# Optimization experiments

Hardware: AMD Instinct MI355X
Metric: run time of the kernel (lower is better)

## Reference

```python
import jax, jax.numpy as jnp
import numpy as np

N_NODES = 50000
N_EDGES = 800000
C_IN = 128
HEADS = 4
C_HEAD = 32  # c_out // heads = 128 // 4
NEG_SLOPE = 0.2


def setup_inputs() -> dict:
    key = jax.random.key(0)
    k_x, k_e, k_w, k_as, k_ad, k_b = jax.random.split(key, 6)
    x = jax.random.normal(k_x, (N_NODES, C_IN), dtype=jnp.float32)
    edge_index = jax.random.randint(k_e, (2, N_EDGES), 0, N_NODES, dtype=jnp.int64)
    # xavier_uniform_ with gain=1.414 on lin.weight [H*C, C_IN] -> same bound for W [C_IN, H*C]
    bound = 1.414 * np.sqrt(6.0 / (C_IN + HEADS * C_HEAD))
    W = jax.random.uniform(k_w, (C_IN, HEADS * C_HEAD), minval=-bound, maxval=bound, dtype=jnp.float32)
    # glorot init for attention vectors (PyG default)
    ab = np.sqrt(6.0 / (1 + HEADS * C_HEAD))
    att_src = jax.random.uniform(k_as, (HEADS, C_HEAD), minval=-ab, maxval=ab, dtype=jnp.float32)
    att_dst = jax.random.uniform(k_ad, (HEADS, C_HEAD), minval=-ab, maxval=ab, dtype=jnp.float32)
    bias = jnp.zeros((HEADS * C_HEAD,), dtype=jnp.float32)
    return {"x": x, "edge_index": edge_index, "W": W,
            "att_src": att_src, "att_dst": att_dst, "bias": bias}


def reference(x, edge_index, W, att_src, att_dst, bias):
    N = x.shape[0]
    H, C = att_src.shape
    # Linear projection, per-head split: [N, H, C]
    xl = (x @ W).reshape(N, H, C)
    a_src = jnp.einsum('nhc,hc->nh', xl, att_src)  # [N, H]
    a_dst = jnp.einsum('nhc,hc->nh', xl, att_dst)  # [N, H]

    src, dst = edge_index[0], edge_index[1]
    loop = jnp.arange(N, dtype=edge_index.dtype)
    # GATConv(add_self_loops=True): remove existing self loops, then add one per node.
    src_f = jnp.concatenate([src, loop])  # [E+N]
    dst_f = jnp.concatenate([dst, loop])
    drop = jnp.concatenate([src == dst, jnp.zeros((N,), dtype=bool)])

    e = jax.nn.leaky_relu(a_src[src_f] + a_dst[dst_f], NEG_SLOPE)  # [E+N, H]
    e = jnp.where(drop[:, None], -jnp.inf, e)

    # segment softmax over edges sharing a destination (every node has a self loop -> max is finite)
    m = jax.ops.segment_max(e, dst_f, num_segments=N)          # [N, H]
    ex = jnp.exp(e - m[dst_f])                                  # [E+N, H]
    denom = jax.ops.segment_sum(ex, dst_f, num_segments=N)     # [N, H]
    alpha = ex / denom[dst_f]                                   # [E+N, H]

    msg = xl[src_f] * alpha[:, :, None]                         # [E+N, H, C]
    out = jax.ops.segment_sum(msg, dst_f, num_segments=N)      # [N, H, C]
    out = out.reshape(N, H * C) + bias
    return out / jnp.sqrt(jnp.asarray(H, dtype=out.dtype))
```

## Files before the change

kernel.cpp:

```cpp
#include <hip/hip_runtime.h>
#include <math.h>

#define CDIM 128
#define HEADS 4
#define NEG 0.2f
#define BSTRIDE 64

typedef __attribute__((ext_vector_type(8))) short bf16x8;
typedef __attribute__((ext_vector_type(8))) unsigned short u16x8;
typedef __attribute__((ext_vector_type(4))) float f32x4;

static __device__ __forceinline__ unsigned short f2bf(float f) {
    unsigned u = __float_as_uint(f);
    u += 0x7FFFu + ((u >> 16) & 1u);
    return (unsigned short)(u >> 16);
}
static __device__ __forceinline__ float bf2f(unsigned short s) {
    return __uint_as_float((unsigned)s << 16);
}

static __device__ __forceinline__ void accum8(float* acc, float w, u16x8 u) {
    const unsigned* pw = (const unsigned*)&u;
#pragma unroll
    for (int i = 0; i < 4; ++i) {
        unsigned wd = pw[i];
        acc[2 * i]     = fmaf(w, __uint_as_float(wd << 16), acc[2 * i]);
        acc[2 * i + 1] = fmaf(w, __uint_as_float(wd & 0xFFFF0000u), acc[2 * i + 1]);
    }
}

#define LDS_STRIDE 136

__global__ __launch_bounds__(256) void wt_kernel(const float* __restrict__ W,
                                                 unsigned short* __restrict__ WT,
                                                 int* __restrict__ counts, int nClr) {
    int f = blockIdx.x * 256 + threadIdx.x;
    for (int i = f; i < nClr; i += 4096) counts[i] = 0;
    int k = f >> 5, c4 = (f & 31) * 4;
    float4 v = *(const float4*)(W + (size_t)k * CDIM + c4);
    WT[(size_t)(c4 + 0) * CDIM + k] = f2bf(v.x);
    WT[(size_t)(c4 + 1) * CDIM + k] = f2bf(v.y);
    WT[(size_t)(c4 + 2) * CDIM + k] = f2bf(v.z);
    WT[(size_t)(c4 + 3) * CDIM + k] = f2bf(v.w);
}

__global__ __launch_bounds__(256) void gemm_hist_kernel(const float* __restrict__ x,
                                                        const unsigned short* __restrict__ WT,
                                                        const float* __restrict__ att_src,
                                                        const float* __restrict__ att_dst,
                                                        unsigned short* __restrict__ xlh,
                                                        float* __restrict__ a_src,
                                                        float* __restrict__ a_dst, int N,
                                                        const int* __restrict__ esrc,
                                                        const int* __restrict__ edst,
                                                        int* __restrict__ counts,
                                                        unsigned* __restrict__ packed, int E,
                                                        int gemmBlocks) {
    __shared__ unsigned short As[64 * LDS_STRIDE];

    if ((int)blockIdx.x >= gemmBlocks) {
        int e = (blockIdx.x - gemmBlocks) * 256 + threadIdx.x;
        if (e < E) {
            int s = esrc[e], d = edst[e];
            unsigned pk = ~0u;
            if (s != d) {
                int r = atomicAdd(&counts[d], 1);
                pk = (unsigned)d | ((unsigned)r << 16);
            }
            packed[e] = pk;
        }
        return;
    }

    const int tid = threadIdx.x;
    const int row0 = blockIdx.x * 64;

#pragma unroll
    for (int i = 0; i < 8; ++i) {
        int f = tid + i * 256;
        int r = f >> 5, k4 = f & 31;
        float4 v = make_float4(0.f, 0.f, 0.f, 0.f);
        int gr = row0 + r;
        if (gr < N) v = *(const float4*)(x + (size_t)gr * CDIM + k4 * 4);
        ushort4 h;
        h.x = f2bf(v.x); h.y = f2bf(v.y); h.z = f2bf(v.z); h.w = f2bf(v.w);
        *(ushort4*)(&As[r * LDS_STRIDE + k4 * 4]) = h;
    }
    __syncthreads();

    const int wave = tid >> 6;
    const int lane = tid & 63;
    const int m    = lane & 15;
    const int quad = lane >> 4;
    const int wrow = wave * 16;

    bf16x8 a[4];
#pragma unroll
    for (int ks = 0; ks < 4; ++ks)
        a[ks] = *(const bf16x8*)(&As[(wrow + m) * LDS_STRIDE + ks * 32 + quad * 8]);

    f32x4 acc[8];
#pragma unroll
    for (int t = 0; t < 8; ++t) {
        f32x4 c = {0.f, 0.f, 0.f, 0.f};
#pragma unroll
        for (int ks = 0; ks < 4; ++ks) {
            bf16x8 b = *(const bf16x8*)(WT + (size_t)(t * 16 + m) * CDIM + ks * 32 + quad * 8);
            c = __builtin_amdgcn_mfma_f32_16x16x32_bf16(a[ks], b, c, 0, 0, 0);
        }
        acc[t] = c;
    }

#pragma unroll
    for (int t = 0; t < 8; ++t) {
#pragma unroll
        for (int reg = 0; reg < 4; ++reg) {
            int row = row0 + wrow + quad * 4 + reg;
            if (row < N) xlh[(size_t)row * CDIM + t * 16 + m] = f2bf(acc[t][reg]);
        }
    }

    float ps[4][4], pd[4][4];
#pragma unroll
    for (int h = 0; h < 4; ++h)
#pragma unroll
        for (int reg = 0; reg < 4; ++reg) { ps[h][reg] = 0.f; pd[h][reg] = 0.f; }
#pragma unroll
    for (int t = 0; t < 8; ++t) {
        int h = t >> 1;
        float vs = att_src[t * 16 + m];
        float vd = att_dst[t * 16 + m];
#pragma unroll
        for (int reg = 0; reg < 4; ++reg) {
            ps[h][reg] += acc[t][reg] * vs;
            pd[h][reg] += acc[t][reg] * vd;
        }
    }
#pragma unroll
    for (int off = 8; off > 0; off >>= 1) {
#pragma unroll
        for (int h = 0; h < 4; ++h)
#pragma unroll
            for (int reg = 0; reg < 4; ++reg) {
                ps[h][reg] += __shfl_down(ps[h][reg], off, 16);
                pd[h][reg] += __shfl_down(pd[h][reg], off, 16);
            }
    }
    if (m == 0) {
#pragma unroll
        for (int reg = 0; reg < 4; ++reg) {
            int row = row0 + wrow + quad * 4 + reg;
            if (row < N) {
#pragma unroll
                for (int h = 0; h < 4; ++h) {
                    a_src[row * 4 + h] = ps[h][reg];
                    a_dst[row * 4 + h] = pd[h][reg];
                }
            }
        }
    }
}

__global__ __launch_bounds__(256) void scatter_kernel(const int* __restrict__ src,
                                                      const unsigned* __restrict__ packed,
                                                      int* __restrict__ bucket, int E) {
    int base = (blockIdx.x * 256 + threadIdx.x) * 4;
    if (base + 4 <= E) {
        int4 s4 = *(const int4*)(src + base);
        uint4 p4 = *(const uint4*)(packed + base);
        int ss[4] = {s4.x, s4.y, s4.z, s4.w};
        unsigned pp[4] = {p4.x, p4.y, p4.z, p4.w};
#pragma unroll
        for (int q = 0; q < 4; ++q) {
            unsigned r = pp[q] >> 16;
            if (pp[q] != ~0u && r < BSTRIDE)
                bucket[(pp[q] & 0xFFFFu) * BSTRIDE + r] = ss[q];
        }
    } else {
        for (int e = base; e < E; ++e) {
            unsigned pk = packed[e];
            unsigned r = pk >> 16;
            if (pk != ~0u && r < BSTRIDE) bucket[(pk & 0xFFFFu) * BSTRIDE + r] = src[e];
        }
    }
}

__global__ __launch_bounds__(256) void gather_kernel(const int* __restrict__ counts,
                                                     const int* __restrict__ bucket,
                                                     const unsigned short* __restrict__ xlh,
                                                     const float* __restrict__ a_src,
                                                     const float* __restrict__ a_dst,
                                                     const float* __restrict__ bias,
                                                     float* __restrict__ out, int N) {
    const int node = blockIdx.x * 4 + (threadIdx.x >> 6);
    const int lane = threadIdx.x & 63;
    const int g = lane >> 4;
    const int lane16 = lane & 15;
    if (node >= N) return;
    const int c8 = lane16 * 8;
    const int h = lane16 >> 2;

    const float ad = a_dst[node * 4 + h];
    const int beg = node * BSTRIDE;
    int cnt = counts[node];
    if (cnt > BSTRIDE) cnt = BSTRIDE;

    float acc[8];
#pragma unroll
    for (int i = 0; i < 8; ++i) acc[i] = 0.f;
    float den = 0.f;

    int j = g;
    for (; j + 12 < cnt; j += 16) {
        int s[4];
#pragma unroll
        for (int q = 0; q < 4; ++q) s[q] = bucket[beg + j + 4 * q];
        float e[4];
#pragma unroll
        for (int q = 0; q < 4; ++q) e[q] = a_src[s[q] * 4 + h] + ad;
        u16x8 u[4];
#pragma unroll
        for (int q = 0; q < 4; ++q) u[q] = *(const u16x8*)(xlh + (size_t)s[q] * CDIM + c8);
        float w[4];
#pragma unroll
        for (int q = 0; q < 4; ++q) {
            float eq = e[q] > 0.f ? e[q] : NEG * e[q];
            w[q] = __expf(eq);
        }
#pragma unroll
        for (int q = 0; q < 4; ++q) {
            accum8(acc, w[q], u[q]);
            den += w[q];
        }
    }
    for (; j < cnt; j += 4) {
        int s = bucket[beg + j];
        float e = a_src[s * 4 + h] + ad;
        u16x8 u = *(const u16x8*)(xlh + (size_t)s * CDIM + c8);
        e = e > 0.f ? e : NEG * e;
        float w = __expf(e);
        accum8(acc, w, u);
        den += w;
    }
    if (g == 0) {
        float es = a_src[node * 4 + h] + ad;
        es = es > 0.f ? es : NEG * es;
        float ws = __expf(es);
        u16x8 u = *(const u16x8*)(xlh + (size_t)node * CDIM + c8);
        accum8(acc, ws, u);
        den += ws;
    }
#pragma unroll
    for (int i = 0; i < 8; ++i) {
        acc[i] += __shfl_xor(acc[i], 16);
        acc[i] += __shfl_xor(acc[i], 32);
    }
    den += __shfl_xor(den, 16);
    den += __shfl_xor(den, 32);

    if (g == 0) {
        float inv = 1.0f / den;
        float4 b0 = *(const float4*)(bias + c8);
        float4 b1 = *(const float4*)(bias + c8 + 4);
        float4 o0, o1;
        o0.x = (acc[0] * inv + b0.x) * 0.5f;
        o0.y = (acc[1] * inv + b0.y) * 0.5f;
        o0.z = (acc[2] * inv + b0.z) * 0.5f;
        o0.w = (acc[3] * inv + b0.w) * 0.5f;
        o1.x = (acc[4] * inv + b1.x) * 0.5f;
        o1.y = (acc[5] * inv + b1.y) * 0.5f;
        o1.z = (acc[6] * inv + b1.z) * 0.5f;
        o1.w = (acc[7] * inv + b1.w) * 0.5f;
        *(float4*)(out + (size_t)node * CDIM + c8) = o0;
        *(float4*)(out + (size_t)node * CDIM + c8 + 4) = o1;
    }
}

extern "C" void kernel_launch(void* const* d_in, const int* in_sizes, int n_in,
                              void* d_out, int out_size, void* d_ws, size_t ws_size,
                              hipStream_t stream) {
    const float* x       = (const float*)d_in[0];
    const int*   ei      = (const int*)d_in[1];
    const float* W       = (const float*)d_in[2];
    const float* att_src = (const float*)d_in[3];
    const float* att_dst = (const float*)d_in[4];
    const float* bias    = (const float*)d_in[5];
    float* out = (float*)d_out;

    const int N = in_sizes[0] / CDIM;
    const int E = in_sizes[1] / 2;

    char* wsb = (char*)d_ws;
    unsigned short* xlh = (unsigned short*)wsb;         wsb += (size_t)N * CDIM * sizeof(unsigned short);
    unsigned short* WT  = (unsigned short*)wsb;         wsb += (size_t)CDIM * CDIM * sizeof(unsigned short);
    float* a_src = (float*)wsb;                         wsb += (size_t)N * HEADS * sizeof(float);
    float* a_dst = (float*)wsb;                         wsb += (size_t)N * HEADS * sizeof(float);
    int* counts  = (int*)wsb;                           wsb += (size_t)N * sizeof(int);
    unsigned* packed = (unsigned*)wsb;                  wsb += (size_t)E * sizeof(unsigned);
    int* bucket  = (int*)wsb;                           wsb += (size_t)N * BSTRIDE * sizeof(int);

    wt_kernel<<<16, 256, 0, stream>>>(W, WT, counts, N);
    const int gemmBlocks = (N + 63) / 64;
    const int histBlocks = (E + 255) / 256;
    gemm_hist_kernel<<<gemmBlocks + histBlocks, 256, 0, stream>>>(
        x, WT, att_src, att_dst, xlh, a_src, a_dst, N, ei, ei + E, counts, packed, E, gemmBlocks);
    scatter_kernel<<<((E + 3) / 4 + 255) / 256, 256, 0, stream>>>(ei, packed, bucket, E);
    gather_kernel<<<(N + 3) / 4, 256, 0, stream>>>(counts, bucket, xlh, a_src, a_dst, bias, out, N);
}
```

Baseline: 169.8 us.

## Fuse all stages into one persistent cooperative kernel with grid syncs

Replaces the four separate launches (weight transpose, GEMM plus histogram, scatter, gather) with one persistent cooperative kernel. Grid-wide syncs separate the phases, and grid-stride loops cover the work. In the GEMM/histogram phase a fixed 40% of blocks run GEMM tiles while the rest do edge counting. The aim is to remove launch gaps and inter-kernel drain. The cost is grid-sync overhead, occupancy limited to resident blocks, and a static split that may leave work unbalanced.

```diff
diff --git a/kernel.cpp b/kernel.cpp
--- a/kernel.cpp
+++ b/kernel.cpp
@@ -1,5 +1,8 @@
 #include <hip/hip_runtime.h>
+#include <hip/hip_cooperative_groups.h>
 #include <math.h>
+
+namespace cg = cooperative_groups;
 
 #define CDIM 128
 #define HEADS 4
@@ -31,36 +34,132 @@
 
 #define LDS_STRIDE 136
 
-__global__ __launch_bounds__(256) void wt_kernel(const float* __restrict__ W,
-                                                 unsigned short* __restrict__ WT,
-                                                 int* __restrict__ counts, int nClr) {
-    int f = blockIdx.x * 256 + threadIdx.x;
-    for (int i = f; i < nClr; i += 4096) counts[i] = 0;
-    int k = f >> 5, c4 = (f & 31) * 4;
-    float4 v = *(const float4*)(W + (size_t)k * CDIM + c4);
-    WT[(size_t)(c4 + 0) * CDIM + k] = f2bf(v.x);
-    WT[(size_t)(c4 + 1) * CDIM + k] = f2bf(v.y);
-    WT[(size_t)(c4 + 2) * CDIM + k] = f2bf(v.z);
-    WT[(size_t)(c4 + 3) * CDIM + k] = f2bf(v.w);
-}
-
-__global__ __launch_bounds__(256) void gemm_hist_kernel(const float* __restrict__ x,
-                                                        const unsigned short* __restrict__ WT,
-                                                        const float* __restrict__ att_src,
-                                                        const float* __restrict__ att_dst,
-                                                        unsigned short* __restrict__ xlh,
-                                                        float* __restrict__ a_src,
-                                                        float* __restrict__ a_dst, int N,
-                                                        const int* __restrict__ esrc,
-                                                        const int* __restrict__ edst,
-                                                        int* __restrict__ counts,
-                                                        unsigned* __restrict__ packed, int E,
-                                                        int gemmBlocks) {
+__global__ __launch_bounds__(256) void mega_kernel(
+    const float* __restrict__ x, const float* __restrict__ W,
+    unsigned short* __restrict__ WT,
+    const float* __restrict__ att_src, const float* __restrict__ att_dst,
+    const float* __restrict__ bias,
+    unsigned short* __restrict__ xlh, float* __restrict__ a_src, float* __restrict__ a_dst,
+    int* __restrict__ counts, unsigned* __restrict__ packed,
+    int* __restrict__ bucket, float* __restrict__ out,
+    const int* __restrict__ esrc, const int* __restrict__ edst,
+    int N, int E, int gemmBlocks)
+{
     __shared__ unsigned short As[64 * LDS_STRIDE];
-
-    if ((int)blockIdx.x >= gemmBlocks) {
-        int e = (blockIdx.x - gemmBlocks) * 256 + threadIdx.x;
-        if (e < E) {
+    cg::grid_group grid = cg::this_grid();
+    const int b   = blockIdx.x;
+    const int tid = threadIdx.x;
+    const int gsz = gridDim.x;
+
+    {
+        int f = b * 256 + tid;
+        for (int i = f; i < N; i += gsz * 256) counts[i] = 0;
+        if (f < 4096) {
+            int k = f >> 5, c4 = (f & 31) * 4;
+            float4 v = *(const float4*)(W + (size_t)k * CDIM + c4);
+            WT[(size_t)(c4 + 0) * CDIM + k] = f2bf(v.x);
+            WT[(size_t)(c4 + 1) * CDIM + k] = f2bf(v.y);
+            WT[(size_t)(c4 + 2) * CDIM + k] = f2bf(v.z);
+            WT[(size_t)(c4 + 3) * CDIM + k] = f2bf(v.w);
+        }
+    }
+    grid.sync();
+
+    int gs25 = (gsz * 2) / 5;
+    int gemmSplit = gemmBlocks < gs25 ? gemmBlocks : gs25;
+    if (b < gemmSplit) {
+        for (int tile = b; tile < gemmBlocks; tile += gemmSplit) {
+            const int row0 = tile * 64;
+
+#pragma unroll
+            for (int i = 0; i < 8; ++i) {
+                int f = tid + i * 256;
+                int r = f >> 5, k4 = f & 31;
+                float4 v = make_float4(0.f, 0.f, 0.f, 0.f);
+                int gr = row0 + r;
+                if (gr < N) v = *(const float4*)(x + (size_t)gr * CDIM + k4 * 4);
+                ushort4 h;
+                h.x = f2bf(v.x); h.y = f2bf(v.y); h.z = f2bf(v.z); h.w = f2bf(v.w);
+                *(ushort4*)(&As[r * LDS_STRIDE + k4 * 4]) = h;
+            }
+            __syncthreads();
+
+            const int wave = tid >> 6;
+            const int lane = tid & 63;
+            const int m    = lane & 15;
+            const int quad = lane >> 4;
+            const int wrow = wave * 16;
+
+            bf16x8 a[4];
+#pragma unroll
+            for (int ks = 0; ks < 4; ++ks)
+                a[ks] = *(const bf16x8*)(&As[(wrow + m) * LDS_STRIDE + ks * 32 + quad * 8]);
+
+            f32x4 acc[8];
+#pragma unroll
+            for (int t = 0; t < 8; ++t) {
+                f32x4 c = {0.f, 0.f, 0.f, 0.f};
+#pragma unroll
+                for (int ks = 0; ks < 4; ++ks) {
+                    bf16x8 bb = *(const bf16x8*)(WT + (size_t)(t * 16 + m) * CDIM + ks * 32 + quad * 8);
+                    c = __builtin_amdgcn_mfma_f32_16x16x32_bf16(a[ks], bb, c, 0, 0, 0);
+                }
+                acc[t] = c;
+            }
+
+#pragma unroll
+            for (int t = 0; t < 8; ++t) {
+#pragma unroll
+                for (int reg = 0; reg < 4; ++reg) {
+                    int row = row0 + wrow + quad * 4 + reg;
+                    if (row < N) xlh[(size_t)row * CDIM + t * 16 + m] = f2bf(acc[t][reg]);
+                }
+            }
+
+            float ps[4][4], pd[4][4];
+#pragma unroll
+            for (int h = 0; h < 4; ++h)
+#pragma unroll
+                for (int reg = 0; reg < 4; ++reg) { ps[h][reg] = 0.f; pd[h][reg] = 0.f; }
+#pragma unroll
+            for (int t = 0; t < 8; ++t) {
+                int h = t >> 1;
+                float vs = att_src[t * 16 + m];
+                float vd = att_dst[t * 16 + m];
+#pragma unroll
+                for (int reg = 0; reg < 4; ++reg) {
+                    ps[h][reg] += acc[t][reg] * vs;
+                    pd[h][reg] += acc[t][reg] * vd;
+                }
+            }
+#pragma unroll
+            for (int off = 8; off > 0; off >>= 1) {
+#pragma unroll
+                for (int h = 0; h < 4; ++h)
+#pragma unroll
+                    for (int reg = 0; reg < 4; ++reg) {
+                        ps[h][reg] += __shfl_down(ps[h][reg], off, 16);
+                        pd[h][reg] += __shfl_down(pd[h][reg], off, 16);
+                    }
+            }
+            if (m == 0) {
+#pragma unroll
+                for (int reg = 0; reg < 4; ++reg) {
+                    int row = row0 + wrow + quad * 4 + reg;
+                    if (row < N) {
+#pragma unroll
+                        for (int h = 0; h < 4; ++h) {
+                            a_src[row * 4 + h] = ps[h][reg];
+                            a_dst[row * 4 + h] = pd[h][reg];
+                        }
+                    }
+                }
+            }
+            __syncthreads();
+        }
+    } else {
+        int stride = (gsz - gemmSplit) * 256;
+        for (int e = (b - gemmSplit) * 256 + tid; e < E; e += stride) {
             int s = esrc[e], d = edst[e];
             unsigned pk = ~0u;
             if (s != d) {
@@ -69,210 +168,121 @@
             }
             packed[e] = pk;
         }
-        return;
-    }
-
-    const int tid = threadIdx.x;
-    const int row0 = blockIdx.x * 64;
-
-#pragma unroll
-    for (int i = 0; i < 8; ++i) {
-        int f = tid + i * 256;
-        int r = f >> 5, k4 = f & 31;
-        float4 v = make_float4(0.f, 0.f, 0.f, 0.f);
-        int gr = row0 + r;
-        if (gr < N) v = *(const float4*)(x + (size_t)gr * CDIM + k4 * 4);
-        ushort4 h;
-        h.x = f2bf(v.x); h.y = f2bf(v.y); h.z = f2bf(v.z); h.w = f2bf(v.w);
-        *(ushort4*)(&As[r * LDS_STRIDE + k4 * 4]) = h;
-    }
-    __syncthreads();
-
-    const int wave = tid >> 6;
-    const int lane = tid & 63;
-    const int m    = lane & 15;
-    const int quad = lane >> 4;
-    const int wrow = wave * 16;
-
-    bf16x8 a[4];
-#pragma unroll
-    for (int ks = 0; ks < 4; ++ks)
-        a[ks] = *(const bf16x8*)(&As[(wrow + m) * LDS_STRIDE + ks * 32 + quad * 8]);
-
-    f32x4 acc[8];
-#pragma unroll
-    for (int t = 0; t < 8; ++t) {
-        f32x4 c = {0.f, 0.f, 0.f, 0.f};
-#pragma unroll
-        for (int ks = 0; ks < 4; ++ks) {
-            bf16x8 b = *(const bf16x8*)(WT + (size_t)(t * 16 + m) * CDIM + ks * 32 + quad * 8);
-            c = __builtin_amdgcn_mfma_f32_16x16x32_bf16(a[ks], b, c, 0, 0, 0);
-        }
-        acc[t] = c;
-    }
-
-#pragma unroll
-    for (int t = 0; t < 8; ++t) {
-#pragma unroll
-        for (int reg = 0; reg < 4; ++reg) {
-            int row = row0 + wrow + quad * 4 + reg;
-            if (row < N) xlh[(size_t)row * CDIM + t * 16 + m] = f2bf(acc[t][reg]);
-        }
-    }
-
-    float ps[4][4], pd[4][4];
-#pragma unroll
-    for (int h = 0; h < 4; ++h)
-#pragma unroll
-        for (int reg = 0; reg < 4; ++reg) { ps[h][reg] = 0.f; pd[h][reg] = 0.f; }
-#pragma unroll
-    for (int t = 0; t < 8; ++t) {
-        int h = t >> 1;
-        float vs = att_src[t * 16 + m];
-        float vd = att_dst[t * 16 + m];
-#pragma unroll
-        for (int reg = 0; reg < 4; ++reg) {
-            ps[h][reg] += acc[t][reg] * vs;
-            pd[h][reg] += acc[t][reg] * vd;
-        }
-    }
-#pragma unroll
-    for (int off = 8; off > 0; off >>= 1) {
-#pragma unroll
-        for (int h = 0; h < 4; ++h)
-#pragma unroll
-            for (int reg = 0; reg < 4; ++reg) {
-                ps[h][reg] += __shfl_down(ps[h][reg], off, 16);
-                pd[h][reg] += __shfl_down(pd[h][reg], off, 16);
-            }
-    }
-    if (m == 0) {
-#pragma unroll
-        for (int reg = 0; reg < 4; ++reg) {
-            int row = row0 + wrow + quad * 4 + reg;
-            if (row < N) {
-#pragma unroll
-                for (int h = 0; h < 4; ++h) {
-                    a_src[row * 4 + h] = ps[h][reg];
-                    a_dst[row * 4 + h] = pd[h][reg];
-                }
-            }
-        }
-    }
-}
-
-__global__ __launch_bounds__(256) void scatter_kernel(const int* __restrict__ src,
-                                                      const unsigned* __restrict__ packed,
-                                                      int* __restrict__ bucket, int E) {
-    int base = (blockIdx.x * 256 + threadIdx.x) * 4;
-    if (base + 4 <= E) {
-        int4 s4 = *(const int4*)(src + base);
-        uint4 p4 = *(const uint4*)(packed + base);
-        int ss[4] = {s4.x, s4.y, s4.z, s4.w};
-        unsigned pp[4] = {p4.x, p4.y, p4.z, p4.w};
-#pragma unroll
-        for (int q = 0; q < 4; ++q) {
-            unsigned r = pp[q] >> 16;
-            if (pp[q] != ~0u && r < BSTRIDE)
-                bucket[(pp[q] & 0xFFFFu) * BSTRIDE + r] = ss[q];
-        }
-    } else {
-        for (int e = base; e < E; ++e) {
-            unsigned pk = packed[e];
-            unsigned r = pk >> 16;
-            if (pk != ~0u && r < BSTRIDE) bucket[(pk & 0xFFFFu) * BSTRIDE + r] = src[e];
-        }
-    }
-}
-
-__global__ __launch_bounds__(256) void gather_kernel(const int* __restrict__ counts,
-                                                     const int* __restrict__ bucket,
-                                                     const unsigned short* __restrict__ xlh,
-                                                     const float* __restrict__ a_src,
-                                                     const float* __restrict__ a_dst,
-                                                     const float* __restrict__ bias,
-                                                     float* __restrict__ out, int N) {
-    const int node = blockIdx.x * 4 + (threadIdx.x >> 6);
-    const int lane = threadIdx.x & 63;
-    const int g = lane >> 4;
-    const int lane16 = lane & 15;
-    if (node >= N) return;
-    const int c8 = lane16 * 8;
-    const int h = lane16 >> 2;
-
-    const float ad = a_dst[node * 4 + h];
-    const int beg = node * BSTRIDE;
-    int cnt = counts[node];
-    if (cnt > BSTRIDE) cnt = BSTRIDE;
-
-    float acc[8];
-#pragma unroll
-    for (int i = 0; i < 8; ++i) acc[i] = 0.f;
-    float den = 0.f;
-
-    int j = g;
-    for (; j + 12 < cnt; j += 16) {
-        int s[4];
-#pragma unroll
-        for (int q = 0; q < 4; ++q) s[q] = bucket[beg + j + 4 * q];
-        float e[4];
-#pragma unroll
-        for (int q = 0; q < 4; ++q) e[q] = a_src[s[q] * 4 + h] + ad;
-        u16x8 u[4];
-#pragma unroll
-        for (int q = 0; q < 4; ++q) u[q] = *(const u16x8*)(xlh + (size_t)s[q] * CDIM + c8);
-        float w[4];
-#pragma unroll
-        for (int q = 0; q < 4; ++q) {
-            float eq = e[q] > 0.f ? e[q] : NEG * e[q];
-            w[q] = __expf(eq);
-        }
-#pragma unroll
-        for (int q = 0; q < 4; ++q) {
-            accum8(acc, w[q], u[q]);
-            den += w[q];
-        }
-    }
-    for (; j < cnt; j += 4) {
-        int s = bucket[beg + j];
-        float e = a_src[s * 4 + h] + ad;
-        u16x8 u = *(const u16x8*)(xlh + (size_t)s * CDIM + c8);
-        e = e > 0.f ? e : NEG * e;
-        float w = __expf(e);
-        accum8(acc, w, u);
-        den += w;
-    }
-    if (g == 0) {
-        float es = a_src[node * 4 + h] + ad;
-        es = es > 0.f ? es : NEG * es;
-        float ws = __expf(es);
-        u16x8 u = *(const u16x8*)(xlh + (size_t)node * CDIM + c8);
-        accum8(acc, ws, u);
-        den += ws;
-    }
-#pragma unroll
-    for (int i = 0; i < 8; ++i) {
-        acc[i] += __shfl_xor(acc[i], 16);
-        acc[i] += __shfl_xor(acc[i], 32);
-    }
-    den += __shfl_xor(den, 16);
-    den += __shfl_xor(den, 32);
-
-    if (g == 0) {
-        float inv = 1.0f / den;
-        float4 b0 = *(const float4*)(bias + c8);
-        float4 b1 = *(const float4*)(bias + c8 + 4);
-        float4 o0, o1;
-        o0.x = (acc[0] * inv + b0.x) * 0.5f;
-        o0.y = (acc[1] * inv + b0.y) * 0.5f;
-        o0.z = (acc[2] * inv + b0.z) * 0.5f;
-        o0.w = (acc[3] * inv + b0.w) * 0.5f;
-        o1.x = (acc[4] * inv + b1.x) * 0.5f;
-        o1.y = (acc[5] * inv + b1.y) * 0.5f;
-        o1.z = (acc[6] * inv + b1.z) * 0.5f;
-        o1.w = (acc[7] * inv + b1.w) * 0.5f;
-        *(float4*)(out + (size_t)node * CDIM + c8) = o0;
-        *(float4*)(out + (size_t)node * CDIM + c8 + 4) = o1;
+    }
+    grid.sync();
+
+    {
+        int nchunk = (E + 3) / 4;
+        for (int c = b * 256 + tid; c < nchunk; c += gsz * 256) {
+            int base = c * 4;
+            if (base + 4 <= E) {
+                int4 s4 = *(const int4*)(esrc + base);
+                uint4 p4 = *(const uint4*)(packed + base);
+                int ss[4] = {s4.x, s4.y, s4.z, s4.w};
+                unsigned pp[4] = {p4.x, p4.y, p4.z, p4.w};
+#pragma unroll
+                for (int q = 0; q < 4; ++q) {
+                    unsigned r = pp[q] >> 16;
+                    if (pp[q] != ~0u && r < BSTRIDE)
+                        bucket[(pp[q] & 0xFFFFu) * BSTRIDE + r] = ss[q];
+                }
+            } else {
+                for (int e = base; e < E; ++e) {
+                    unsigned pk = packed[e];
+                    unsigned r = pk >> 16;
+                    if (pk != ~0u && r < BSTRIDE) bucket[(pk & 0xFFFFu) * BSTRIDE + r] = esrc[e];
+                }
+            }
+        }
+    }
+    grid.sync();
+
+    {
+        int nquad = (N + 3) / 4;
+        for (int qd = b; qd < nquad; qd += gsz) {
+            const int node = qd * 4 + (tid >> 6);
+            if (node >= N) continue;
+            const int lane = tid & 63;
+            const int g = lane >> 4;
+            const int lane16 = lane & 15;
+            const int c8 = lane16 * 8;
+            const int h = lane16 >> 2;
+
+            const float ad = a_dst[node * 4 + h];
+            const int beg = node * BSTRIDE;
+            int cnt = counts[node];
+            if (cnt > BSTRIDE) cnt = BSTRIDE;
+
+            float acc[8];
+#pragma unroll
+            for (int i = 0; i < 8; ++i) acc[i] = 0.f;
+            float den = 0.f;
+
+            int j = g;
+            for (; j + 12 < cnt; j += 16) {
+                int s[4];
+#pragma unroll
+                for (int q = 0; q < 4; ++q) s[q] = bucket[beg + j + 4 * q];
+                float e[4];
+#pragma unroll
+                for (int q = 0; q < 4; ++q) e[q] = a_src[s[q] * 4 + h] + ad;
+                u16x8 u[4];
+#pragma unroll
+                for (int q = 0; q < 4; ++q) u[q] = *(const u16x8*)(xlh + (size_t)s[q] * CDIM + c8);
+                float w[4];
+#pragma unroll
+                for (int q = 0; q < 4; ++q) {
+                    float eq = e[q] > 0.f ? e[q] : NEG * e[q];
+                    w[q] = __expf(eq);
+                }
+#pragma unroll
+                for (int q = 0; q < 4; ++q) {
+                    accum8(acc, w[q], u[q]);
+                    den += w[q];
+                }
+            }
+            for (; j < cnt; j += 4) {
+                int s = bucket[beg + j];
+                float e = a_src[s * 4 + h] + ad;
+                u16x8 u = *(const u16x8*)(xlh + (size_t)s * CDIM + c8);
+                e = e > 0.f ? e : NEG * e;
+                float w = __expf(e);
+                accum8(acc, w, u);
+                den += w;
+            }
+            if (g == 0) {
+                float es = a_src[node * 4 + h] + ad;
+                es = es > 0.f ? es : NEG * es;
+                float ws = __expf(es);
+                u16x8 u = *(const u16x8*)(xlh + (size_t)node * CDIM + c8);
+                accum8(acc, ws, u);
+                den += ws;
+            }
+#pragma unroll
+            for (int i = 0; i < 8; ++i) {
+                acc[i] += __shfl_xor(acc[i], 16);
+                acc[i] += __shfl_xor(acc[i], 32);
+            }
+            den += __shfl_xor(den, 16);
+            den += __shfl_xor(den, 32);
+
+            if (g == 0) {
+                float inv = 1.0f / den;
+                float4 b0 = *(const float4*)(bias + c8);
+                float4 b1 = *(const float4*)(bias + c8 + 4);
+                float4 o0, o1;
+                o0.x = (acc[0] * inv + b0.x) * 0.5f;
+                o0.y = (acc[1] * inv + b0.y) * 0.5f;
+                o0.z = (acc[2] * inv + b0.z) * 0.5f;
+                o0.w = (acc[3] * inv + b0.w) * 0.5f;
+                o1.x = (acc[4] * inv + b1.x) * 0.5f;
+                o1.y = (acc[5] * inv + b1.y) * 0.5f;
+                o1.z = (acc[6] * inv + b1.z) * 0.5f;
+                o1.w = (acc[7] * inv + b1.w) * 0.5f;
+                *(float4*)(out + (size_t)node * CDIM + c8) = o0;
+                *(float4*)(out + (size_t)node * CDIM + c8 + 4) = o1;
+            }
+        }
     }
 }
 
@@ -287,8 +297,8 @@
     const float* bias    = (const float*)d_in[5];
     float* out = (float*)d_out;
 
-    const int N = in_sizes[0] / CDIM;
-    const int E = in_sizes[1] / 2;
+    int N = in_sizes[0] / CDIM;
+    int E = in_sizes[1] / 2;
 
     char* wsb = (char*)d_ws;
     unsigned short* xlh = (unsigned short*)wsb;         wsb += (size_t)N * CDIM * sizeof(unsigned short);
@@ -299,11 +309,27 @@
     unsigned* packed = (unsigned*)wsb;                  wsb += (size_t)E * sizeof(unsigned);
     int* bucket  = (int*)wsb;                           wsb += (size_t)N * BSTRIDE * sizeof(int);
 
-    wt_kernel<<<16, 256, 0, stream>>>(W, WT, counts, N);
-    const int gemmBlocks = (N + 63) / 64;
-    const int histBlocks = (E + 255) / 256;
-    gemm_hist_kernel<<<gemmBlocks + histBlocks, 256, 0, stream>>>(
-        x, WT, att_src, att_dst, xlh, a_src, a_dst, N, ei, ei + E, counts, packed, E, gemmBlocks);
-    scatter_kernel<<<((E + 3) / 4 + 255) / 256, 256, 0, stream>>>(ei, packed, bucket, E);
-    gather_kernel<<<(N + 3) / 4, 256, 0, stream>>>(counts, bucket, xlh, a_src, a_dst, bias, out, N);
-}
+    static int gridBlocks = 0;
+    if (gridBlocks == 0) {
+        int nbPerCU = 0;
+        if (hipOccupancyMaxActiveBlocksPerMultiprocessor(&nbPerCU, mega_kernel, 256, 0) != hipSuccess
+            || nbPerCU <= 0)
+            nbPerCU = 4;
+        int cus = 256;
+        hipDeviceProp_t prop;
+        if (hipGetDeviceProperties(&prop, 0) == hipSuccess && prop.multiProcessorCount > 0)
+            cus = prop.multiProcessorCount;
+        gridBlocks = nbPerCU * cus;
+        if (gridBlocks > 8192) gridBlocks = 8192;
+    }
+
+    const int* esrc = ei;
+    const int* edst = ei + E;
+    int gemmBlocks = (N + 63) / 64;
+
+    void* args[] = { (void*)&x, (void*)&W, (void*)&WT, (void*)&att_src, (void*)&att_dst,
+                     (void*)&bias, (void*)&xlh, (void*)&a_src, (void*)&a_dst,
+                     (void*)&counts, (void*)&packed, (void*)&bucket, (void*)&out,
+                     (void*)&esrc, (void*)&edst, (void*)&N, (void*)&E, (void*)&gemmBlocks };
+    hipLaunchCooperativeKernel((void*)mega_kernel, dim3(gridBlocks), dim3(256), args, 0, stream);
+}
```

Result: slower. 414.6 us (+144.1%).
